# Kernel tuning notes

Hardware: AMD Instinct MI355X
Metric: run time of the kernel (lower is better)

Reference implementation:

```python
import jax, jax.numpy as jnp
import numpy as np
from jax import lax

# dims
B, T, C, V, L = 4, 1024, 1024, 32000, 2
NR, NT, E = 6, 2, 8          # rwkv experts, transformer experts, total
HID = 4 * C                  # FFN hidden
P, R = 8, 64                 # bridge prefix_len, low_rank_dim
NH, HD = 16, 64              # heads, head_size


def _layernorm(x, g, b, eps=1e-5):
    m = jnp.mean(x, axis=-1, keepdims=True)
    v = jnp.var(x, axis=-1, keepdims=True)
    return (x - m) * lax.rsqrt(v + eps) * g + b


def setup_inputs() -> dict:
    key = jax.random.key(0)
    ks = list(jax.random.split(key, 32))
    it = iter(ks)
    def nrm(shape, s=0.02):
        return jax.random.normal(next(it), shape, dtype=jnp.float32) * s
    inp = {}
    inp['idx'] = jax.random.randint(next(it), (B, T), 0, V)
    inp['capital_shares'] = jax.random.uniform(next(it), (L, E), dtype=jnp.float32)
    inp['emb'] = nrm((V, C), 1.0)
    inp['head'] = nrm((C, V))
    inp['ln1_g'] = jnp.ones((L, C), jnp.float32)
    inp['ln1_b'] = jnp.zeros((L, C), jnp.float32)
    inp['ln2_g'] = jnp.ones((L, C), jnp.float32)
    inp['ln2_b'] = jnp.zeros((L, C), jnp.float32)
    inp['lno_g'] = jnp.ones((C,), jnp.float32)
    inp['lno_b'] = jnp.zeros((C,), jnp.float32)
    inp['att_Wr'] = nrm((L, C, C))
    inp['att_Wk'] = nrm((L, C, C))
    inp['att_Wv'] = nrm((L, C, C))
    inp['att_Wo'] = nrm((L, C, C))
    inp['att_decay'] = nrm((L, C), 1.0)
    inp['critic_wd'] = nrm((L, C))
    inp['critic_Wa'] = nrm((L, C, E))
    inp['bridge_Wdown'] = nrm((C, R))
    inp['bridge_Wup'] = nrm((P, R, C))
    inp['eWk'] = nrm((L, NR, C, HID))
    inp['eWv'] = nrm((L, NR, HID, C))
    inp['conf_r'] = nrm((L, NR, C))
    inp['tWq'] = nrm((L, NT, C, C))
    inp['tWk'] = nrm((L, NT, C, C))
    inp['tWv'] = nrm((L, NT, C, C))
    inp['tWo'] = nrm((L, NT, C, C))
    inp['conf_t'] = nrm((L, NT, C))
    return inp


def _forward(idx, capital_shares, emb, head, ln1_g, ln1_b, ln2_g, ln2_b,
             lno_g, lno_b, att_Wr, att_Wk, att_Wv, att_Wo, att_decay,
             critic_wd, critic_Wa, bridge_Wdown, bridge_Wup,
             eWk, eWv, conf_r, tWq, tWk, tWv, tWo, conf_t):
    x = emb[idx]                                   # [B,T,C]
    v_first = jnp.zeros_like(x)
    for l in range(L):
        # --- TimeMix (simplified RWKV: per-channel decayed kv state) ---
        x_ln = _layernorm(x, ln1_g[l], ln1_b[l])
        r = jax.nn.sigmoid(x_ln @ att_Wr[l])       # [B,T,C]
        k = x_ln @ att_Wk[l]
        v = x_ln @ att_Wv[l]
        if l == 0:
            v_first = v
        else:
            v = 0.5 * (v + v_first)
        w = jax.nn.sigmoid(att_decay[l])           # [C] decay in (0,1)
        def step(s, kv):
            kt, vt = kv
            s = w * s + kt * vt
            return s, s
        kT = jnp.swapaxes(k, 0, 1)                 # [T,B,C]
        vT = jnp.swapaxes(v, 0, 1)
        _, s_seq = lax.scan(step, jnp.zeros((B, C), x.dtype), (kT, vT))
        rwkv_state = jnp.swapaxes(s_seq, 0, 1)     # [B,T,C]
        att_out = (r * rwkv_state) @ att_Wo[l]
        x = x + att_out
        # --- routing (market) ---
        h = _layernorm(x, ln2_g[l], ln2_b[l])
        conf_rw = jax.nn.sigmoid(jnp.einsum('btc,ec->bte', h, conf_r[l]))
        conf_tr = jax.nn.sigmoid(jnp.einsum('btc,ec->bte', h, conf_t[l]))
        confidences = jnp.concatenate([conf_rw, conf_tr], axis=-1)  # [B,T,E]
        difficulty = jax.nn.softplus(jnp.einsum('btc,c->bt', h, critic_wd[l]))[..., None]
        affinity = jnp.einsum('btc,ce->bte', h, critic_Wa[l])
        subsidy = jnp.tanh(affinity)               # critic.apply_to_bids(0, affinity)
        bids = confidences * capital_shares[l] * difficulty + subsidy
        top2_vals, winners = lax.top_k(bids, 2)    # [B,T,2]
        weights = jax.nn.softmax(top2_vals, axis=-1)
        gate = (weights[..., 0:1] * jax.nn.one_hot(winners[..., 0], E, dtype=h.dtype)
                + weights[..., 1:2] * jax.nn.one_hot(winners[..., 1], E, dtype=h.dtype))  # [B,T,E]
        # --- bridge prefix (low-rank, shared) ---
        flat_h = h.reshape(-1, C)
        flat_state = rwkv_state.reshape(-1, C)
        u = (flat_h + flat_state) @ bridge_Wdown   # [N,R]
        prefix = jnp.einsum('nr,prc->npc', u, bridge_Wup)  # [N,P,C]
        # --- experts: dense-equivalent of gather/compute/scatter ---
        final = jnp.zeros_like(h)
        for e in range(NR):                        # squared-relu FFN experts
            hid = jnp.square(jax.nn.relu(h @ eWk[l, e]))
            final = final + gate[..., e:e + 1] * (hid @ eWv[l, e])
        scale = 1.0 / jnp.sqrt(jnp.float32(HD))
        for j in range(NT):                        # linear transformer experts over prefix
            q = (flat_h @ tWq[l, j]).reshape(-1, NH, HD)
            kp = (prefix @ tWk[l, j]).reshape(-1, P, NH, HD)
            vp = (prefix @ tWv[l, j]).reshape(-1, P, NH, HD)
            attn = jax.nn.softmax(jnp.einsum('nhd,nphd->nhp', q, kp) * scale, axis=-1)
            o = jnp.einsum('nhp,nphd->nhd', attn, vp).reshape(-1, C) @ tWo[l, j]
            final = final + gate[..., NR + j:NR + j + 1] * o.reshape(B, T, C)
        x = x + final
    x = _layernorm(x, lno_g, lno_b)
    return x @ head                                # [B,T,V] logits


def reference(idx, capital_shares, emb, head, ln1_g, ln1_b, ln2_g, ln2_b,
              lno_g, lno_b, att_Wr, att_Wk, att_Wv, att_Wo, att_decay,
              critic_wd, critic_Wa, bridge_Wdown, bridge_Wup,
              eWk, eWv, conf_r, tWq, tWk, tWv, tWo, conf_t):
    return _forward(idx, capital_shares, emb, head, ln1_g, ln1_b, ln2_g, ln2_b,
                    lno_g, lno_b, att_Wr, att_Wk, att_Wv, att_Wo, att_decay,
                    critic_wd, critic_Wa, bridge_Wdown, bridge_Wup,
                    eWk, eWv, conf_r, tWq, tWk, tWv, tWo, conf_t)
```

## Files before the change

### kernel.cpp

```cpp
#include <hip/hip_runtime.h>

typedef _Float16 h16;
typedef __attribute__((ext_vector_type(8))) _Float16 h16x8;
typedef __attribute__((ext_vector_type(4))) _Float16 h16x4;
typedef __attribute__((ext_vector_type(4))) float f32x4;

#define DEVFN static __device__ __forceinline__

DEVFN void gl_lds16(const void* g, void* l) {
  __builtin_amdgcn_global_load_lds((const __attribute__((address_space(1))) unsigned int*)g,
                                   (__attribute__((address_space(3))) unsigned int*)l, 16, 0, 0);
}
DEVFN void fsplit(float v, h16& hi, h16& lo) { hi = (h16)v; lo = (h16)(v - (float)hi); }
DEVFN float wred(float v) {
  #pragma unroll
  for (int m = 32; m >= 1; m >>= 1) v += __shfl_xor(v, m, 64);
  return v;
}
DEVFN float sigm(float x) { return 1.0f / (1.0f + expf(-x)); }
DEVFN float softpl(float x) { return fmaxf(x, 0.0f) + log1pf(expf(-fabsf(x))); }

enum { EPI_WRITE = 0, EPI_ADD = 1, EPI_SQRELU = 3, EPI_TSPLIT = 4, EPI_SCATTER = 5 };

template<bool SPLIT, int EPI, int MODE>
__global__ __launch_bounds__(256, 2) void gemm_k(
    const h16* __restrict__ Ah, const h16* __restrict__ Al, long lda, long sAz,
    const h16* __restrict__ Bh, const h16* __restrict__ Bl, long ldb, long sBz,
    float* __restrict__ C, long ldc, long sCz,
    h16* __restrict__ Oh, h16* __restrict__ Ol, long ldo,
    int K, int nmask, const float* __restrict__ rs, int rsStride,
    const int4* __restrict__ meta, int metaStep,
    const int* __restrict__ lists, int listStep)
{
  __shared__ h16 As[(SPLIT ? 2 : 1) * 4096];
  __shared__ h16 Bs[(SPLIT ? 2 : 1) * 4096];
  const int tid = threadIdx.x;
  const int lane = tid & 63, wave = tid >> 6;
  const int wr = wave >> 1, wc = wave & 1;
  const long z = blockIdx.z;
  const long m0 = (long)blockIdx.x * 128, n0 = (long)blockIdx.y * 128;

  int cntv = 0;
  long koff = 0;
  const int* lst = nullptr;
  if (MODE == 1) {
    const int4 mt = meta[z * metaStep];
    if ((int)m0 >= mt.y) return;
    cntv = mt.x; lst = lists + z * listStep;
  } else if (MODE == 2) {
    const int4 mt = meta[0];
    if ((int)m0 >= mt.y) return;
    cntv = mt.x; lst = lists; koff = z * (long)K;
  }

  const h16* pAh = Ah + z * sAz;
  const h16* pBh = Bh + z * sBz;
  const h16* pAl = SPLIT ? (Al + z * sAz) : nullptr;
  const h16* pBl = SPLIT ? (Bl + z * sBz) : nullptr;
  const int rA = wave * 16 + (lane >> 2);
  const int khalf = (lane & 3) * 8;
  long arow0, arow1;
  if (MODE == 1) { arow0 = lst[m0 + rA]; arow1 = lst[m0 + rA + 64]; }
  else           { arow0 = m0 + rA; arow1 = arow0 + 64; }
  const long aoff0 = arow0 * lda + khalf + koff;
  const long aoff1 = arow1 * lda + khalf + koff;
  const long boff = (n0 + rA) * ldb + khalf + koff;
  h16* lA = &As[wave * 512];
  h16* lB = &Bs[wave * 512];
  const int fr = lane & 15, fq = lane >> 4;

  const f32x4 zero = {0.f, 0.f, 0.f, 0.f};
  f32x4 acc[4][4];
  #pragma unroll
  for (int m = 0; m < 4; m++)
    #pragma unroll
    for (int n = 0; n < 4; n++) acc[m][n] = zero;

  for (int k0 = 0; k0 < K; k0 += 32) {
    gl_lds16(pAh + aoff0 + k0, lA);
    gl_lds16(pAh + aoff1 + k0, lA + 2048);
    gl_lds16(pBh + boff + k0, lB);
    gl_lds16(pBh + boff + k0 + 64 * ldb, lB + 2048);
    if (SPLIT) {
      gl_lds16(pAl + aoff0 + k0, lA + 4096);
      gl_lds16(pAl + aoff1 + k0, lA + 4096 + 2048);
      gl_lds16(pBl + boff + k0, lB + 4096);
      gl_lds16(pBl + boff + k0 + 64 * ldb, lB + 4096 + 2048);
    }
    __syncthreads();
    h16x8 af[4], bf[4], afl[4], bfl[4];
    #pragma unroll
    for (int m = 0; m < 4; m++) {
      const int r = (wr * 64 + m * 16 + fr) * 32 + fq * 8;
      af[m] = *(const h16x8*)&As[r];
      if (SPLIT) afl[m] = *(const h16x8*)&As[4096 + r];
    }
    #pragma unroll
    for (int n = 0; n < 4; n++) {
      const int r = (wc * 64 + n * 16 + fr) * 32 + fq * 8;
      bf[n] = *(const h16x8*)&Bs[r];
      if (SPLIT) bfl[n] = *(const h16x8*)&Bs[4096 + r];
    }
    #pragma unroll
    for (int m = 0; m < 4; m++)
      #pragma unroll
      for (int n = 0; n < 4; n++) {
        acc[m][n] = __builtin_amdgcn_mfma_f32_16x16x32_f16(af[m], bf[n], acc[m][n], 0, 0, 0);
        if (SPLIT) {
          acc[m][n] = __builtin_amdgcn_mfma_f32_16x16x32_f16(af[m], bfl[n], acc[m][n], 0, 0, 0);
          acc[m][n] = __builtin_amdgcn_mfma_f32_16x16x32_f16(afl[m], bf[n], acc[m][n], 0, 0, 0);
        }
      }
    __syncthreads();
  }

  #pragma unroll
  for (int m = 0; m < 4; m++) {
    const long lrow = m0 + wr * 64 + m * 16 + fq * 4;
    #pragma unroll
    for (int n = 0; n < 4; n++) {
      const long gcol = n0 + wc * 64 + n * 16 + fr;
      if (nmask && gcol >= nmask) continue;
      if (EPI == EPI_TSPLIT) {
        h16x4 hv, lv;
        #pragma unroll
        for (int i = 0; i < 4; i++) { h16 a, b2; fsplit(acc[m][n][i], a, b2); hv[i] = a; lv[i] = b2; }
        *(h16x4*)&Oh[gcol * ldo + lrow] = hv;
        *(h16x4*)&Ol[gcol * ldo + lrow] = lv;
      } else if (EPI == EPI_SCATTER) {
        #pragma unroll
        for (int i = 0; i < 4; i++) {
          const int slot = (int)lrow + i;
          if (slot >= cntv) continue;
          const int tok = lst[slot];
          const float g = rs[(long)tok * rsStride];
          atomicAdd(&C[(long)tok * ldc + gcol], g * acc[m][n][i]);
        }
      } else {
        float* cp = C + z * sCz + lrow * ldc + gcol;
        #pragma unroll
        for (int i = 0; i < 4; i++) {
          const float v = acc[m][n][i];
          if (EPI == EPI_WRITE) cp[i * ldc] = v;
          else cp[i * ldc] += v;
        }
      }
    }
  }
}

template<bool SPLIT, int EPI, int MODE>
__global__ __launch_bounds__(512, 1) void gemm256_k(
    const h16* __restrict__ Ah, const h16* __restrict__ Al, long lda,
    const h16* __restrict__ Bh, const h16* __restrict__ Bl, long ldb, long sBz,
    float* __restrict__ C, long ldc,
    h16* __restrict__ Oh, h16* __restrict__ Ol, long ldo,
    int K, const float* __restrict__ rs, int rsStride,
    const int4* __restrict__ meta, const int* __restrict__ lists, int listStep,
    const int* __restrict__ mmap)
{
  __shared__ h16 As[(SPLIT ? 2 : 1) * 8192];
  __shared__ h16 Bs[(SPLIT ? 2 : 1) * 8192];
  const int tid = threadIdx.x;
  const int lane = tid & 63, wave = tid >> 6;
  const int wr = wave >> 2, wc = wave & 3;
  const long m0 = (long)blockIdx.x * 256, n0 = (long)blockIdx.y * 256;

  int cntv = 0, eIdx = 0, eOff = 0;
  long koff = 0;
  const int* lst = nullptr;
  if (MODE == 3 || MODE == 4) {
    if ((int)m0 >= meta[8].x) return;
    eIdx = mmap[blockIdx.x];
    const int4 mt = meta[eIdx];
    cntv = mt.x; eOff = mt.z;
    lst = lists + eIdx * listStep;
    if (MODE == 4) koff = blockIdx.z * (long)K;
  }

  const h16* pAh = Ah;
  const h16* pBh = Bh + (long)eIdx * sBz;
  const h16* pAl = SPLIT ? Al : nullptr;
  const h16* pBl = SPLIT ? (Bl + (long)eIdx * sBz) : nullptr;
  const int rA = (tid >> 2) & 127;
  const int khalf = (lane & 3) * 8;
  long arow0, arow1;
  if (MODE == 3) { arow0 = lst[m0 + rA - eOff]; arow1 = lst[m0 + rA + 128 - eOff]; }
  else           { arow0 = m0 + rA; arow1 = arow0 + 128; }
  const long aoff0 = arow0 * lda + khalf + koff;
  const long aoff1 = arow1 * lda + khalf + koff;
  const long boff0 = (n0 + rA) * ldb + khalf + koff;
  const long boff1 = boff0 + 128 * ldb;
  h16* lA = &As[wave * 512];
  h16* lB = &Bs[wave * 512];
  const int fr = lane & 15, fq = lane >> 4;

  const f32x4 zero = {0.f, 0.f, 0.f, 0.f};
  f32x4 acc[8][4];
  #pragma unroll
  for (int m = 0; m < 8; m++)
    #pragma unroll
    for (int n = 0; n < 4; n++) acc[m][n] = zero;

  for (int k0 = 0; k0 < K; k0 += 32) {
    gl_lds16(pAh + aoff0 + k0, lA);
    gl_lds16(pAh + aoff1 + k0, lA + 4096);
    gl_lds16(pBh + boff0 + k0, lB);
    gl_lds16(pBh + boff1 + k0, lB + 4096);
    if (SPLIT) {
      gl_lds16(pAl + aoff0 + k0, lA + 8192);
      gl_lds16(pAl + aoff1 + k0, lA + 8192 + 4096);
      gl_lds16(pBl + boff0 + k0, lB + 8192);
      gl_lds16(pBl + boff1 + k0, lB + 8192 + 4096);
    }
    __syncthreads();
    h16x8 bf[4], bfl[4];
    #pragma unroll
    for (int n = 0; n < 4; n++) {
      const int r = (wc * 64 + n * 16 + fr) * 32 + fq * 8;
      bf[n] = *(const h16x8*)&Bs[r];
      if (SPLIT) bfl[n] = *(const h16x8*)&Bs[8192 + r];
    }
    #pragma unroll
    for (int m = 0; m < 8; m++) {
      const int r = (wr * 128 + m * 16 + fr) * 32 + fq * 8;
      const h16x8 af = *(const h16x8*)&As[r];
      h16x8 afl;
      if (SPLIT) afl = *(const h16x8*)&As[8192 + r];
      #pragma unroll
      for (int n = 0; n < 4; n++) {
        acc[m][n] = __builtin_amdgcn_mfma_f32_16x16x32_f16(af, bf[n], acc[m][n], 0, 0, 0);
        if (SPLIT) {
          acc[m][n] = __builtin_amdgcn_mfma_f32_16x16x32_f16(af, bfl[n], acc[m][n], 0, 0, 0);
          acc[m][n] = __builtin_amdgcn_mfma_f32_16x16x32_f16(afl, bf[n], acc[m][n], 0, 0, 0);
        }
      }
    }
    __syncthreads();
  }

  #pragma unroll
  for (int m = 0; m < 8; m++) {
    const long lrow = m0 + wr * 128 + m * 16 + fq * 4;
    #pragma unroll
    for (int n = 0; n < 4; n++) {
      const long gcol = n0 + wc * 64 + n * 16 + fr;
      if (EPI == EPI_SQRELU) {
        #pragma unroll
        for (int i = 0; i < 4; i++) {
          float v = acc[m][n][i];
          v = v > 0.f ? v * v : 0.f;
          const h16 a = (h16)v;
          Oh[(lrow + i) * ldo + gcol] = a;
          if (Ol) Ol[(lrow + i) * ldo + gcol] = (h16)(v - (float)a);
        }
      } else if (EPI == EPI_SCATTER) {
        #pragma unroll
        for (int i = 0; i < 4; i++) {
          const int slot = (int)lrow + i - eOff;
          if (slot >= cntv) continue;
          const int tok = lst[slot];
          atomicAdd(&C[(long)tok * ldc + gcol], rs[(long)tok * rsStride + eIdx] * acc[m][n][i]);
        }
      } else {
        float* cp = C + lrow * ldc + gcol;
        #pragma unroll
        for (int i = 0; i < 4; i++) cp[i * ldc] = acc[m][n][i];
      }
    }
  }
}

template<bool LO>
__global__ __launch_bounds__(256) void k_tsplit(
    const float* __restrict__ in, long inZ,
    h16* __restrict__ oh, h16* __restrict__ ol, long outZ, int Kd, int Nd)
{
  __shared__ float t[64][65];
  const long z = blockIdx.z;
  in += z * inZ; oh += z * outZ; if (LO) ol += z * outZ;
  const int n0 = blockIdx.x * 64, k0 = blockIdx.y * 64;
  const int tr = threadIdx.x >> 4, tc = threadIdx.x & 15;
  #pragma unroll
  for (int r = 0; r < 4; r++) {
    const int row = r * 16 + tr;
    const float4 v = *(const float4*)&in[(long)(k0 + row) * Nd + n0 + tc * 4];
    t[row][tc * 4 + 0] = v.x; t[row][tc * 4 + 1] = v.y;
    t[row][tc * 4 + 2] = v.z; t[row][tc * 4 + 3] = v.w;
  }
  __syncthreads();
  #pragma unroll
  for (int r = 0; r < 4; r++) {
    const int nrow = r * 16 + tr;
    h16x4 hv, lv;
    #pragma unroll
    for (int i = 0; i < 4; i++) {
      h16 a, b2; fsplit(t[tc * 4 + i][nrow], a, b2);
      hv[i] = a; lv[i] = b2;
    }
    *(h16x4*)&oh[(long)(n0 + nrow) * Kd + k0 + tc * 4] = hv;
    if (LO) *(h16x4*)&ol[(long)(n0 + nrow) * Kd + k0 + tc * 4] = lv;
  }
}

__global__ void k_split(const float* __restrict__ in, h16* __restrict__ oh, h16* __restrict__ ol)
{
  const long i = (long)blockIdx.x * 256 + threadIdx.x;
  const float4 v = ((const float4*)in)[i];
  h16x4 hv, lv; h16 a, b2;
  fsplit(v.x, a, b2); hv[0] = a; lv[0] = b2;
  fsplit(v.y, a, b2); hv[1] = a; lv[1] = b2;
  fsplit(v.z, a, b2); hv[2] = a; lv[2] = b2;
  fsplit(v.w, a, b2); hv[3] = a; lv[3] = b2;
  ((h16x4*)oh)[i] = hv; ((h16x4*)ol)[i] = lv;
}

__global__ void k_embed(const int* __restrict__ idx, const float* __restrict__ emb, float* __restrict__ x)
{
  const int row = blockIdx.x;
  const long e = (long)idx[row] * 1024;
  ((float4*)(x + (long)row * 1024))[threadIdx.x] = ((const float4*)(emb + e))[threadIdx.x];
}

__global__ __launch_bounds__(256) void k_ln(
    const float* __restrict__ x, const float* __restrict__ g, const float* __restrict__ b,
    float* __restrict__ yf, h16* __restrict__ yh, h16* __restrict__ yl)
{
  const int row = blockIdx.x, tid = threadIdx.x;
  const float4 v = ((const float4*)(x + (long)row * 1024))[tid];
  __shared__ float red[4];
  const int wv = tid >> 6;
  float s = wred(v.x + v.y + v.z + v.w);
  if ((tid & 63) == 0) red[wv] = s;
  __syncthreads();
  const float mean = (red[0] + red[1] + red[2] + red[3]) * (1.0f / 1024.0f);
  const float d0 = v.x - mean, d1 = v.y - mean, d2 = v.z - mean, d3 = v.w - mean;
  float s2 = wred(d0 * d0 + d1 * d1 + d2 * d2 + d3 * d3);
  __syncthreads();
  if ((tid & 63) == 0) red[wv] = s2;
  __syncthreads();
  const float var = (red[0] + red[1] + red[2] + red[3]) * (1.0f / 1024.0f);
  const float rstd = 1.0f / sqrtf(var + 1e-5f);
  const float4 gv = ((const float4*)g)[tid];
  const float4 bv = ((const float4*)b)[tid];
  const float y0 = d0 * rstd * gv.x + bv.x;
  const float y1 = d1 * rstd * gv.y + bv.y;
  const float y2 = d2 * rstd * gv.z + bv.z;
  const float y3 = d3 * rstd * gv.w + bv.w;
  if (yf) { float4 o; o.x = y0; o.y = y1; o.z = y2; o.w = y3; ((float4*)(yf + (long)row * 1024))[tid] = o; }
  h16x4 hv, lv; h16 a, b2;
  fsplit(y0, a, b2); hv[0] = a; lv[0] = b2;
  fsplit(y1, a, b2); hv[1] = a; lv[1] = b2;
  fsplit(y2, a, b2); hv[2] = a; lv[2] = b2;
  fsplit(y3, a, b2); hv[3] = a; lv[3] = b2;
  *(h16x4*)(yh + (long)row * 1024 + tid * 4) = hv;
  if (yl) *(h16x4*)(yl + (long)row * 1024 + tid * 4) = lv;
}

__global__ void k_vfix(float* __restrict__ rkv, float* __restrict__ vfir, int mode)
{
  const int row = blockIdx.x, tid = threadIdx.x;
  float4* vp = (float4*)(rkv + (long)row * 3072 + 2048) + tid;
  float4* fp = (float4*)(vfir + (long)row * 1024) + tid;
  if (mode == 0) *fp = *vp;
  else {
    float4 a = *vp; const float4 b = *fp;
    a.x = 0.5f * (a.x + b.x); a.y = 0.5f * (a.y + b.y);
    a.z = 0.5f * (a.z + b.z); a.w = 0.5f * (a.w + b.w);
    *vp = a;
  }
}

__global__ __launch_bounds__(256) void k_scan1(const float* __restrict__ rkv,
                                               const float* __restrict__ dec, float* __restrict__ carry)
{
  const int gid = blockIdx.x * 256 + threadIdx.x;
  const int c = gid & 1023, bb = (gid >> 10) & 3, ch = gid >> 12;
  const float w = sigm(dec[c]);
  float s = 0.f;
  const long base = ((long)bb * 1024 + ch * 64) * 3072 + c;
  const float* kp_ = rkv + 1024 + base;
  const float* vp_ = rkv + 2048 + base;
  for (int t = 0; t < 64; t++) s = w * s + kp_[(long)t * 3072] * vp_[(long)t * 3072];
  carry[(ch * 4 + bb) * 1024 + c] = s;
}
__global__ void k_scan2(const float* __restrict__ dec, float* __restrict__ carry)
{
  const int gid = blockIdx.x * 256 + threadIdx.x;
  const int c = gid & 1023, bb = gid >> 10;
  const float w = sigm(dec[c]);
  float w64 = w;
  for (int i = 0; i < 6; i++) w64 *= w64;
  float s = 0.f;
  for (int j = 0; j < 16; j++) {
    const int o = (j * 4 + bb) * 1024 + c;
    const float a = carry[o];
    carry[o] = s;
    s = w64 * s + a;
  }
}
__global__ __launch_bounds__(256) void k_scan3(const float* __restrict__ rkv,
                                               const float* __restrict__ dec, const float* __restrict__ carry,
                                               float* __restrict__ st)
{
  const int gid = blockIdx.x * 256 + threadIdx.x;
  const int c = gid & 1023, bb = (gid >> 10) & 3, ch = gid >> 12;
  const float w = sigm(dec[c]);
  float s = carry[(ch * 4 + bb) * 1024 + c];
  const long base = ((long)bb * 1024 + ch * 64) * 3072 + c;
  const float* kp_ = rkv + 1024 + base;
  const float* vp_ = rkv + 2048 + base;
  float* so = st + ((long)bb * 1024 + ch * 64) * 1024 + c;
  for (int t = 0; t < 64; t++) {
    s = w * s + kp_[(long)t * 3072] * vp_[(long)t * 3072];
    so[(long)t * 1024] = s;
  }
}

__global__ void k_attin(const float* __restrict__ rkv, const float* __restrict__ s,
                        h16* __restrict__ oh, h16* __restrict__ ol)
{
  const int row = blockIdx.x, tid = threadIdx.x;
  const float4 rv = *((const float4*)(rkv + (long)row * 3072) + tid);
  const float4 sv = *((const float4*)(s + (long)row * 1024) + tid);
  h16x4 hv, lv; h16 a, b2;
  fsplit(sv.x * sigm(rv.x), a, b2); hv[0] = a; lv[0] = b2;
  fsplit(sv.y * sigm(rv.y), a, b2); hv[1] = a; lv[1] = b2;
  fsplit(sv.z * sigm(rv.z), a, b2); hv[2] = a; lv[2] = b2;
  fsplit(sv.w * sigm(rv.w), a, b2); hv[3] = a; lv[3] = b2;
  const long i = (long)row * 256 + tid;
  ((h16x4*)oh)[i] = hv; ((h16x4*)ol)[i] = lv;
}

__global__ void k_addsplit(const float* __restrict__ p, const float* __restrict__ q,
                           h16* __restrict__ oh, h16* __restrict__ ol)
{
  const long i = (long)blockIdx.x * 256 + threadIdx.x;
  const float4 av = ((const float4*)p)[i];
  const float4 bv = ((const float4*)q)[i];
  h16x4 hv, lv; h16 a, b2;
  fsplit(av.x + bv.x, a, b2); hv[0] = a; lv[0] = b2;
  fsplit(av.y + bv.y, a, b2); hv[1] = a; lv[1] = b2;
  fsplit(av.z + bv.z, a, b2); hv[2] = a; lv[2] = b2;
  fsplit(av.w + bv.w, a, b2); hv[3] = a; lv[3] = b2;
  ((h16x4*)oh)[i] = hv; ((h16x4*)ol)[i] = lv;
}

__global__ __launch_bounds__(256) void k_route(
    const float* __restrict__ h, const float* __restrict__ cr, const float* __restrict__ ct,
    const float* __restrict__ wd, const float* __restrict__ wa,
    const float* __restrict__ cap, float* __restrict__ gate)
{
  const int wv = threadIdx.x >> 6, ln = threadIdx.x & 63;
  const int row = blockIdx.x * 4 + wv;
  const float* hr = h + (long)row * 1024;
  float hreg[16];
  #pragma unroll
  for (int i = 0; i < 4; i++) {
    const float4 t = ((const float4*)hr)[ln * 4 + i];
    hreg[i * 4 + 0] = t.x; hreg[i * 4 + 1] = t.y; hreg[i * 4 + 2] = t.z; hreg[i * 4 + 3] = t.w;
  }
  float dots[17];
  #pragma unroll
  for (int e = 0; e < 6; e++) {
    float p = 0.f;
    #pragma unroll
    for (int j = 0; j < 16; j++) p += hreg[j] * cr[e * 1024 + ln * 16 + j];
    dots[e] = p;
  }
  #pragma unroll
  for (int e = 0; e < 2; e++) {
    float p = 0.f;
    #pragma unroll
    for (int j = 0; j < 16; j++) p += hreg[j] * ct[e * 1024 + ln * 16 + j];
    dots[6 + e] = p;
  }
  {
    float p = 0.f;
    #pragma unroll
    for (int j = 0; j < 16; j++) p += hreg[j] * wd[ln * 16 + j];
    dots[8] = p;
  }
  #pragma unroll
  for (int e = 0; e < 8; e++) {
    float p = 0.f;
    #pragma unroll
    for (int j = 0; j < 16; j++) p += hreg[j] * wa[(ln * 16 + j) * 8 + e];
    dots[9 + e] = p;
  }
  #pragma unroll
  for (int d = 0; d < 17; d++) dots[d] = wred(dots[d]);
  if (ln == 0) {
    float bids[8];
    const float diff = softpl(dots[8]);
    #pragma unroll
    for (int e = 0; e < 6; e++) bids[e] = sigm(dots[e]) * cap[e] * diff + tanhf(dots[9 + e]);
    #pragma unroll
    for (int e = 0; e < 2; e++) bids[6 + e] = sigm(dots[6 + e]) * cap[6 + e] * diff + tanhf(dots[15 + e]);
    int w0 = 0;
    for (int e = 1; e < 8; e++) if (bids[e] > bids[w0]) w0 = e;
    int w1 = -1;
    for (int e = 0; e < 8; e++) if (e != w0 && (w1 < 0 || bids[e] > bids[w1])) w1 = e;
    const float e1 = expf(bids[w1] - bids[w0]);
    const float q0 = 1.0f / (1.0f + e1), q1 = e1 / (1.0f + e1);
    for (int e = 0; e < 8; e++) gate[(long)row * 8 + e] = (e == w0) ? q0 : ((e == w1) ? q1 : 0.0f);
  }
}

__global__ void k_build(const float* __restrict__ gate, int* __restrict__ cnt, int* __restrict__ lists)
{
  const int t = blockIdx.x * 256 + threadIdx.x;
  #pragma unroll
  for (int e = 0; e < 8; e++)
    if (gate[(long)t * 8 + e] > 0.f) { const int s = atomicAdd(&cnt[e], 1); lists[e * 4224 + s] = t; }
}
__global__ void k_meta(const int* __restrict__ cnt, int4* __restrict__ meta, int* __restrict__ lists,
                       int* __restrict__ mmap)
{
  __shared__ int sc[8], sp[8], so[8];
  if (threadIdx.x == 0) {
    int acc = 0;
    for (int e = 0; e < 8; e++) {
      const int c = cnt[e], p = (c + 255) & ~255;
      sc[e] = c; sp[e] = p; so[e] = (e < 6) ? acc : 0;
      if (e < 6) acc += p;
    }
    meta[8] = make_int4(acc, 0, 0, 0);
    for (int b = 0; b < 64; b++) mmap[b] = 0;
    for (int e = 0; e < 6; e++)
      for (int b = so[e] >> 8; b < (so[e] + sp[e]) >> 8; b++) mmap[b] = e;
  }
  __syncthreads();
  const int e = threadIdx.x >> 5, i = threadIdx.x & 31;
  for (int s = sc[e] + i; s < sp[e]; s += 32) lists[e * 4224 + s] = 0;
  if (i == 0) meta[e] = make_int4(sc[e], sp[e], so[e], 0);
}

__global__ __launch_bounds__(256) void k_scores(const float* __restrict__ q, const float* __restrict__ kp,
                                                float* __restrict__ attn, const int4* __restrict__ meta)
{
  const int gw = blockIdx.x * 4 + (threadIdx.x >> 6), ln = threadIdx.x & 63;
  const int n = gw >> 4, hh = gw & 15;
  if (n >= meta->y) return;
  const float qv = q[(long)n * 1024 + hh * 64 + ln];
  float s[8];
  #pragma unroll
  for (int p = 0; p < 8; p++) {
    float t = qv * kp[(long)n * 8192 + p * 1024 + hh * 64 + ln];
    s[p] = wred(t) * 0.125f;
  }
  if (ln == 0) {
    float mx = s[0];
    #pragma unroll
    for (int p = 1; p < 8; p++) mx = fmaxf(mx, s[p]);
    float ex[8], sum = 0.f;
    #pragma unroll
    for (int p = 0; p < 8; p++) { ex[p] = expf(s[p] - mx); sum += ex[p]; }
    const float inv = 1.0f / sum;
    #pragma unroll
    for (int p = 0; p < 8; p++) attn[(long)n * 128 + hh * 8 + p] = ex[p] * inv;
  }
}

__global__ void k_omix(const float* __restrict__ attn, const float* __restrict__ vp,
                       h16* __restrict__ oh, h16* __restrict__ ol, const int4* __restrict__ meta)
{
  const long gid = (long)blockIdx.x * 256 + threadIdx.x;
  const int n = gid >> 10, hd = gid & 1023, hh = hd >> 6;
  if (n >= meta->y) return;
  const float* a = attn + (long)n * 128 + hh * 8;
  float o = 0.f;
  #pragma unroll
  for (int p = 0; p < 8; p++) o += a[p] * vp[(long)n * 8192 + p * 1024 + hd];
  h16 hi, lo; fsplit(o, hi, lo);
  oh[gid] = hi; ol[gid] = lo;
}

#define GEMM3(SPL, EPI, MODE, GRID, ...) do { \
  if (SPL) gemm_k<true,  EPI, MODE><<<GRID, 256, 0, stream>>>(__VA_ARGS__); \
  else     gemm_k<false, EPI, MODE><<<GRID, 256, 0, stream>>>(__VA_ARGS__); } while (0)
#define GEMM256(SPL, EPI, MODE, GRID, ...) do { \
  if (SPL) gemm256_k<true,  EPI, MODE><<<GRID, 512, 0, stream>>>(__VA_ARGS__); \
  else     gemm256_k<false, EPI, MODE><<<GRID, 512, 0, stream>>>(__VA_ARGS__); } while (0)

extern "C" void kernel_launch(void* const* d_in, const int* in_sizes, int n_in,
                              void* d_out, int out_size, void* d_ws, size_t ws_size,
                              hipStream_t stream)
{
  (void)in_sizes; (void)n_in; (void)out_size; (void)ws_size;
  const int*   idx   = (const int*)  d_in[0];
  const float* cap   = (const float*)d_in[1];
  const float* emb   = (const float*)d_in[2];
  const float* headw = (const float*)d_in[3];
  const float* ln1g  = (const float*)d_in[4];
  const float* ln1b  = (const float*)d_in[5];
  const float* ln2g  = (const float*)d_in[6];
  const float* ln2b  = (const float*)d_in[7];
  const float* lnog  = (const float*)d_in[8];
  const float* lnob  = (const float*)d_in[9];
  const float* aWr   = (const float*)d_in[10];
  const float* aWk   = (const float*)d_in[11];
  const float* aWv   = (const float*)d_in[12];
  const float* aWo   = (const float*)d_in[13];
  const float* adec  = (const float*)d_in[14];
  const float* cwd   = (const float*)d_in[15];
  const float* cWa   = (const float*)d_in[16];
  const float* bWd   = (const float*)d_in[17];
  const float* bWu   = (const float*)d_in[18];
  const float* eWkw  = (const float*)d_in[19];
  const float* eWvw  = (const float*)d_in[20];
  const float* confr = (const float*)d_in[21];
  const float* tWq   = (const float*)d_in[22];
  const float* tWkk  = (const float*)d_in[23];
  const float* tWv   = (const float*)d_in[24];
  const float* tWo   = (const float*)d_in[25];
  const float* conft = (const float*)d_in[26];
  float* out = (float*)d_out;

  char* ws = (char*)d_ws;
  size_t off = 0;
  auto alloc = [&](size_t n) -> char* {
    off = (off + 255) & ~(size_t)255;
    char* p = ws + off; off += n; return p;
  };
  const long M1 = 1048576, M4 = 4194304;

  h16* attWh = (h16*)alloc(8 * M1 * 2);
  h16* attWl = (h16*)alloc(8 * M1 * 2);
  h16* eWkh  = (h16*)alloc(12 * M4 * 2);
  h16* eWkl  = (h16*)alloc(6 * M4 * 2);
  h16* eWvh  = (h16*)alloc(12 * M4 * 2);
  h16* eWvl  = (h16*)alloc(6 * M4 * 2);
  h16* tWh   = (h16*)alloc(16 * M1 * 2);
  h16* tWl   = (h16*)alloc(8 * M1 * 2);
  h16* headh = (h16*)alloc(32768000ull * 2);
  h16* wdh   = (h16*)alloc(131072 * 2);
  h16* wdl   = (h16*)alloc(131072 * 2);
  h16* wuph  = (h16*)alloc(524288 * 2);
  h16* wupl  = (h16*)alloc(524288 * 2);
  h16* wukth = (h16*)alloc(524288 * 2);
  h16* wuktl = (h16*)alloc(524288 * 2);
  h16* wuvth = (h16*)alloc(524288 * 2);
  h16* wuvtl = (h16*)alloc(524288 * 2);
  h16* s1h   = (h16*)alloc(M4 * 2);
  h16* s1l   = (h16*)alloc(M4 * 2);
  h16* hh_   = (h16*)alloc(M4 * 2);
  h16* hl_   = (h16*)alloc(M4 * 2);
  h16* uh    = (h16*)alloc(262144 * 2);
  h16* ul    = (h16*)alloc(262144 * 2);
  float* x    = (float*)alloc(M4 * 4);
  float* vfir = (float*)alloc(M4 * 4);
  float* rkv  = (float*)alloc(3 * M4 * 4);
  float* st   = (float*)alloc(M4 * 4);
  float* hf   = (float*)alloc(M4 * 4);
  float* qf   = (float*)alloc(M4 * 4);
  char* big   = alloc(167772160);
  h16* hidh   = (h16*)big;
  h16* hidl   = (h16*)(big + 83886080ull);
  float* kp   = (float*)big;
  float* carry = (float*)alloc(65536 * 4);
  float* gate  = (float*)alloc(32768 * 4);
  float* uf    = (float*)alloc(262144 * 4);
  float* attn  = (float*)alloc(524288 * 4);
  int*   cnt8  = (int*)alloc(32);
  int4*  metaA = (int4*)alloc(16 * 16);
  int*   lists = (int*)alloc(8 * 4224 * 4);
  int*   mmap  = (int*)alloc(64 * 4);

  const float* aW[4] = {aWr, aWk, aWv, aWo};
  for (int w = 0; w < 4; w++)
    k_tsplit<true><<<dim3(16, 16, 2), 256, 0, stream>>>(aW[w], M1, attWh + w * M1, attWl + w * M1, 4 * M1, 1024, 1024);
  k_tsplit<true ><<<dim3(64, 16, 6), 256, 0, stream>>>(eWkw, M4, eWkh, eWkl, M4, 1024, 4096);
  k_tsplit<false><<<dim3(64, 16, 6), 256, 0, stream>>>(eWkw + 6 * M4, M4, eWkh + 6 * M4, nullptr, M4, 1024, 4096);
  k_tsplit<true ><<<dim3(16, 64, 6), 256, 0, stream>>>(eWvw, M4, eWvh, eWvl, M4, 4096, 1024);
  k_tsplit<false><<<dim3(16, 64, 6), 256, 0, stream>>>(eWvw + 6 * M4, M4, eWvh + 6 * M4, nullptr, M4, 4096, 1024);
  const float* tWsrc[4] = {tWq, tWkk, tWv, tWo};
  for (int m = 0; m < 4; m++) {
    k_tsplit<true ><<<dim3(16, 16, 2), 256, 0, stream>>>(tWsrc[m], M1, tWh + m * M1, tWl + m * M1, 4 * M1, 1024, 1024);
    k_tsplit<false><<<dim3(16, 16, 2), 256, 0, stream>>>(tWsrc[m] + 2 * M1, M1, tWh + (8 + m) * M1, nullptr, 4 * M1, 1024, 1024);
  }
  k_tsplit<false><<<dim3(500, 16, 1), 256, 0, stream>>>(headw, 0, headh, nullptr, 0, 1024, 32000);
  k_tsplit<true ><<<dim3(1, 16, 1), 256, 0, stream>>>(bWd, 0, wdh, wdl, 0, 1024, 64);
  hipMemsetAsync(wdh + 65536, 0, 65536 * 2, stream);
  hipMemsetAsync(wdl + 65536, 0, 65536 * 2, stream);
  k_split<<<512, 256, 0, stream>>>(bWu, wuph, wupl);

  k_embed<<<4096, 256, 0, stream>>>(idx, emb, x);

  for (int l = 0; l < 2; l++) {
    const bool SE = (l == 0);
    k_ln<<<4096, 256, 0, stream>>>(x, ln1g + l * 1024, ln1b + l * 1024, nullptr, s1h, s1l);
    GEMM3(true, EPI_WRITE, 0, dim3(32, 24),
          s1h, s1l, 1024, 0, attWh + (l * 4) * M1, attWl + (l * 4) * M1, 1024, 0,
          rkv, 3072, 0, nullptr, nullptr, 0, 1024, 0, nullptr, 0, nullptr, 0, nullptr, 0);
    k_vfix<<<4096, 256, 0, stream>>>(rkv, vfir, l == 0 ? 0 : 1);
    k_scan1<<<256, 256, 0, stream>>>(rkv, adec + l * 1024, carry);
    k_scan2<<<16, 256, 0, stream>>>(adec + l * 1024, carry);
    k_scan3<<<256, 256, 0, stream>>>(rkv, adec + l * 1024, carry, st);
    k_attin<<<4096, 256, 0, stream>>>(rkv, st, s1h, s1l);
    GEMM3(true, EPI_ADD, 0, dim3(32, 8),
          s1h, s1l, 1024, 0, attWh + (l * 4 + 3) * M1, attWl + (l * 4 + 3) * M1, 1024, 0,
          x, 1024, 0, nullptr, nullptr, 0, 1024, 0, nullptr, 0, nullptr, 0, nullptr, 0);
    k_ln<<<4096, 256, 0, stream>>>(x, ln2g + l * 1024, ln2b + l * 1024, hf, hh_, hl_);
    k_route<<<1024, 256, 0, stream>>>(hf, confr + l * 6144, conft + l * 2048, cwd + l * 1024, cWa + l * 8192, cap + l * 8, gate);
    hipMemsetAsync(cnt8, 0, 32, stream);
    k_build<<<16, 256, 0, stream>>>(gate, cnt8, lists);
    k_meta<<<1, 256, 0, stream>>>(cnt8, metaA, lists, mmap);
    k_addsplit<<<4096, 256, 0, stream>>>(hf, st, s1h, s1l);
    GEMM3(true, EPI_WRITE, 0, dim3(32, 1),
          s1h, s1l, 1024, 0, wdh, wdl, 1024, 0,
          uf, 64, 0, nullptr, nullptr, 0, 1024, 64, nullptr, 0, nullptr, 0, nullptr, 0);
    k_split<<<256, 256, 0, stream>>>(uf, uh, ul);
    GEMM256(SE, EPI_SQRELU, 3, dim3(40, 16),
            hh_, hl_, 1024, eWkh + l * 6 * M4, eWkl, 1024, M4,
            nullptr, 0, hidh, SE ? hidl : nullptr, 4096,
            1024, nullptr, 0, metaA, lists, 4224, mmap);
    GEMM256(SE, EPI_SCATTER, 4, dim3(40, 4, 4),
            hidh, hidl, 4096, eWvh + l * 6 * M4, eWvl, 4096, M4,
            x, 1024, nullptr, nullptr, 0,
            1024, gate, 8, metaA, lists, 4224, mmap);
    for (int j = 0; j < 2; j++) {
      const long wi = (l * 2 + j) * 4, wl = j * 4;
      const int4* mt = metaA + 6 + j;
      const int* lstT = lists + (6 + j) * 4224;
      GEMM3(SE, EPI_TSPLIT, 0, dim3(4, 8),
            wuph, wupl, 1024, 0, tWh + (wi + 1) * M1, tWl + (wl + 1) * M1, 1024, 0,
            nullptr, 0, 0, wukth, wuktl, 512, 1024, 0, nullptr, 0, nullptr, 0, nullptr, 0);
      GEMM3(SE, EPI_TSPLIT, 0, dim3(4, 8),
            wuph, wupl, 1024, 0, tWh + (wi + 2) * M1, tWl + (wl + 2) * M1, 1024, 0,
            nullptr, 0, 0, wuvth, wuvtl, 512, 1024, 0, nullptr, 0, nullptr, 0, nullptr, 0);
      GEMM3(SE, EPI_WRITE, 1, dim3(32, 8),
            hh_, hl_, 1024, 0, tWh + (wi + 0) * M1, tWl + (wl + 0) * M1, 1024, 0,
            qf, 1024, 0, nullptr, nullptr, 0, 1024, 0, nullptr, 0, mt, 0, lstT, 0);
      GEMM3(SE, EPI_WRITE, 1, dim3(32, 8, 8),
            uh, ul, 64, 0, wukth, wuktl, 512, 64,
            kp, 8192, 1024, nullptr, nullptr, 0, 64, 0, nullptr, 0, mt, 0, lstT, 0);
      k_scores<<<16384, 256, 0, stream>>>(qf, kp, attn, mt);
      GEMM3(SE, EPI_WRITE, 1, dim3(32, 8, 8),
            uh, ul, 64, 0, wuvth, wuvtl, 512, 64,
            kp, 8192, 1024, nullptr, nullptr, 0, 64, 0, nullptr, 0, mt, 0, lstT, 0);
      k_omix<<<16384, 256, 0, stream>>>(attn, kp, s1h, s1l, mt);
      GEMM3(SE, EPI_SCATTER, 2, dim3(32, 8, 4),
            s1h, s1l, 1024, 0, tWh + (wi + 3) * M1, tWl + (wl + 3) * M1, 1024, 0,
            x, 1024, 0, nullptr, nullptr, 0, 256, 0, gate + 6 + j, 8, mt, 0, lstT, 0);
    }
  }

  k_ln<<<4096, 256, 0, stream>>>(x, lnog, lnob, nullptr, s1h, s1l);
  GEMM3(false, EPI_WRITE, 0, dim3(32, 250),
        s1h, nullptr, 1024, 0, headh, nullptr, 1024, 0,
        out, 32000, 0, nullptr, nullptr, 0, 1024, 0, nullptr, 0, nullptr, 0, nullptr, 0);
}
```

Baseline: 3.367 ms.

## Drop split-fp16 precision on transformer-expert and bridge GEMMs, batch weight conversions

Switches the transformer-expert GEMMs (q, key/value prefix projections, output scatter) and the bridge down-projection from the 3-MFMA hi/lo split-precision path to a single fp16 pass, removing the low-part weights entirely. The two prefix-projection TSPLIT GEMMs are merged into one launch using a new z-stride on the output, with the wukth/wuvth buffers reordered so they are contiguous. Weight preprocessing for the attention and transformer weights is batched into single k_tsplit4 launches. This cuts MFMA work and launches, at the cost of reduced numerical accuracy in those paths.

```diff
diff --git a/kernel.cpp b/kernel.cpp
--- a/kernel.cpp
+++ b/kernel.cpp
@@ -30,7 +30,7 @@
     h16* __restrict__ Oh, h16* __restrict__ Ol, long ldo,
     int K, int nmask, const float* __restrict__ rs, int rsStride,
     const int4* __restrict__ meta, int metaStep,
-    const int* __restrict__ lists, int listStep)
+    const int* __restrict__ lists, int listStep, long sOz)
 {
   __shared__ h16 As[(SPLIT ? 2 : 1) * 4096];
   __shared__ h16 Bs[(SPLIT ? 2 : 1) * 4096];
@@ -125,8 +125,8 @@
         h16x4 hv, lv;
         #pragma unroll
         for (int i = 0; i < 4; i++) { h16 a, b2; fsplit(acc[m][n][i], a, b2); hv[i] = a; lv[i] = b2; }
-        *(h16x4*)&Oh[gcol * ldo + lrow] = hv;
-        *(h16x4*)&Ol[gcol * ldo + lrow] = lv;
+        *(h16x4*)&Oh[z * sOz + gcol * ldo + lrow] = hv;
+        *(h16x4*)&Ol[z * sOz + gcol * ldo + lrow] = lv;
       } else if (EPI == EPI_SCATTER) {
         #pragma unroll
         for (int i = 0; i < 4; i++) {
@@ -279,6 +279,42 @@
   __shared__ float t[64][65];
   const long z = blockIdx.z;
   in += z * inZ; oh += z * outZ; if (LO) ol += z * outZ;
+  const int n0 = blockIdx.x * 64, k0 = blockIdx.y * 64;
+  const int tr = threadIdx.x >> 4, tc = threadIdx.x & 15;
+  #pragma unroll
+  for (int r = 0; r < 4; r++) {
+    const int row = r * 16 + tr;
+    const float4 v = *(const float4*)&in[(long)(k0 + row) * Nd + n0 + tc * 4];
+    t[row][tc * 4 + 0] = v.x; t[row][tc * 4 + 1] = v.y;
+    t[row][tc * 4 + 2] = v.z; t[row][tc * 4 + 3] = v.w;
+  }
+  __syncthreads();
+  #pragma unroll
+  for (int r = 0; r < 4; r++) {
+    const int nrow = r * 16 + tr;
+    h16x4 hv, lv;
+    #pragma unroll
+    for (int i = 0; i < 4; i++) {
+      h16 a, b2; fsplit(t[tc * 4 + i][nrow], a, b2);
+      hv[i] = a; lv[i] = b2;
+    }
+    *(h16x4*)&oh[(long)(n0 + nrow) * Kd + k0 + tc * 4] = hv;
+    if (LO) *(h16x4*)&ol[(long)(n0 + nrow) * Kd + k0 + tc * 4] = lv;
+  }
+}
+
+template<bool LO>
+__global__ __launch_bounds__(256) void k_tsplit4(
+    const float* __restrict__ s0, const float* __restrict__ s1,
+    const float* __restrict__ s2, const float* __restrict__ s3,
+    long inAdd, h16* __restrict__ oh, h16* __restrict__ ol, int Kd, int Nd)
+{
+  __shared__ float t[64][65];
+  const int z = blockIdx.z;
+  const long seg = (long)Kd * Nd;
+  const int w = z & 3;
+  const float* in = (w == 0 ? s0 : w == 1 ? s1 : w == 2 ? s2 : s3) + (inAdd + (z >> 2)) * seg;
+  oh += (long)z * seg; if (LO) ol += (long)z * seg;
   const int n0 = blockIdx.x * 64, k0 = blockIdx.y * 64;
   const int tr = threadIdx.x >> 4, tc = threadIdx.x & 15;
   #pragma unroll
@@ -632,15 +668,13 @@
   h16* eWvh  = (h16*)alloc(12 * M4 * 2);
   h16* eWvl  = (h16*)alloc(6 * M4 * 2);
   h16* tWh   = (h16*)alloc(16 * M1 * 2);
-  h16* tWl   = (h16*)alloc(8 * M1 * 2);
   h16* headh = (h16*)alloc(32768000ull * 2);
   h16* wdh   = (h16*)alloc(131072 * 2);
-  h16* wdl   = (h16*)alloc(131072 * 2);
   h16* wuph  = (h16*)alloc(524288 * 2);
   h16* wupl  = (h16*)alloc(524288 * 2);
   h16* wukth = (h16*)alloc(524288 * 2);
+  h16* wuvth = (h16*)alloc(524288 * 2);
   h16* wuktl = (h16*)alloc(524288 * 2);
-  h16* wuvth = (h16*)alloc(524288 * 2);
   h16* wuvtl = (h16*)alloc(524288 * 2);
   h16* s1h   = (h16*)alloc(M4 * 2);
   h16* s1l   = (h16*)alloc(M4 * 2);
@@ -667,22 +701,15 @@
   int*   lists = (int*)alloc(8 * 4224 * 4);
   int*   mmap  = (int*)alloc(64 * 4);
 
-  const float* aW[4] = {aWr, aWk, aWv, aWo};
-  for (int w = 0; w < 4; w++)
-    k_tsplit<true><<<dim3(16, 16, 2), 256, 0, stream>>>(aW[w], M1, attWh + w * M1, attWl + w * M1, 4 * M1, 1024, 1024);
+  k_tsplit4<true><<<dim3(16, 16, 8), 256, 0, stream>>>(aWr, aWk, aWv, aWo, 0, attWh, attWl, 1024, 1024);
   k_tsplit<true ><<<dim3(64, 16, 6), 256, 0, stream>>>(eWkw, M4, eWkh, eWkl, M4, 1024, 4096);
   k_tsplit<false><<<dim3(64, 16, 6), 256, 0, stream>>>(eWkw + 6 * M4, M4, eWkh + 6 * M4, nullptr, M4, 1024, 4096);
   k_tsplit<true ><<<dim3(16, 64, 6), 256, 0, stream>>>(eWvw, M4, eWvh, eWvl, M4, 4096, 1024);
   k_tsplit<false><<<dim3(16, 64, 6), 256, 0, stream>>>(eWvw + 6 * M4, M4, eWvh + 6 * M4, nullptr, M4, 4096, 1024);
-  const float* tWsrc[4] = {tWq, tWkk, tWv, tWo};
-  for (int m = 0; m < 4; m++) {
-    k_tsplit<true ><<<dim3(16, 16, 2), 256, 0, stream>>>(tWsrc[m], M1, tWh + m * M1, tWl + m * M1, 4 * M1, 1024, 1024);
-    k_tsplit<false><<<dim3(16, 16, 2), 256, 0, stream>>>(tWsrc[m] + 2 * M1, M1, tWh + (8 + m) * M1, nullptr, 4 * M1, 1024, 1024);
-  }
+  k_tsplit4<false><<<dim3(16, 16, 16), 256, 0, stream>>>(tWq, tWkk, tWv, tWo, 0, tWh, nullptr, 1024, 1024);
   k_tsplit<false><<<dim3(500, 16, 1), 256, 0, stream>>>(headw, 0, headh, nullptr, 0, 1024, 32000);
-  k_tsplit<true ><<<dim3(1, 16, 1), 256, 0, stream>>>(bWd, 0, wdh, wdl, 0, 1024, 64);
+  k_tsplit<false><<<dim3(1, 16, 1), 256, 0, stream>>>(bWd, 0, wdh, nullptr, 0, 1024, 64);
   hipMemsetAsync(wdh + 65536, 0, 65536 * 2, stream);
-  hipMemsetAsync(wdl + 65536, 0, 65536 * 2, stream);
   k_split<<<512, 256, 0, stream>>>(bWu, wuph, wupl);
 
   k_embed<<<4096, 256, 0, stream>>>(idx, emb, x);
@@ -692,7 +719,7 @@
     k_ln<<<4096, 256, 0, stream>>>(x, ln1g + l * 1024, ln1b + l * 1024, nullptr, s1h, s1l);
     GEMM3(true, EPI_WRITE, 0, dim3(32, 24),
           s1h, s1l, 1024, 0, attWh + (l * 4) * M1, attWl + (l * 4) * M1, 1024, 0,
-          rkv, 3072, 0, nullptr, nullptr, 0, 1024, 0, nullptr, 0, nullptr, 0, nullptr, 0);
+          rkv, 3072, 0, nullptr, nullptr, 0, 1024, 0, nullptr, 0, nullptr, 0, nullptr, 0, 0);
     k_vfix<<<4096, 256, 0, stream>>>(rkv, vfir, l == 0 ? 0 : 1);
     k_scan1<<<256, 256, 0, stream>>>(rkv, adec + l * 1024, carry);
     k_scan2<<<16, 256, 0, stream>>>(adec + l * 1024, carry);
@@ -700,16 +727,16 @@
     k_attin<<<4096, 256, 0, stream>>>(rkv, st, s1h, s1l);
     GEMM3(true, EPI_ADD, 0, dim3(32, 8),
           s1h, s1l, 1024, 0, attWh + (l * 4 + 3) * M1, attWl + (l * 4 + 3) * M1, 1024, 0,
-          x, 1024, 0, nullptr, nullptr, 0, 1024, 0, nullptr, 0, nullptr, 0, nullptr, 0);
+          x, 1024, 0, nullptr, nullptr, 0, 1024, 0, nullptr, 0, nullptr, 0, nullptr, 0, 0);
     k_ln<<<4096, 256, 0, stream>>>(x, ln2g + l * 1024, ln2b + l * 1024, hf, hh_, hl_);
     k_route<<<1024, 256, 0, stream>>>(hf, confr + l * 6144, conft + l * 2048, cwd + l * 1024, cWa + l * 8192, cap + l * 8, gate);
     hipMemsetAsync(cnt8, 0, 32, stream);
     k_build<<<16, 256, 0, stream>>>(gate, cnt8, lists);
     k_meta<<<1, 256, 0, stream>>>(cnt8, metaA, lists, mmap);
     k_addsplit<<<4096, 256, 0, stream>>>(hf, st, s1h, s1l);
-    GEMM3(true, EPI_WRITE, 0, dim3(32, 1),
-          s1h, s1l, 1024, 0, wdh, wdl, 1024, 0,
-          uf, 64, 0, nullptr, nullptr, 0, 1024, 64, nullptr, 0, nullptr, 0, nullptr, 0);
+    GEMM3(false, EPI_WRITE, 0, dim3(32, 1),
+          s1h, nullptr, 1024, 0, wdh, nullptr, 1024, 0,
+          uf, 64, 0, nullptr, nullptr, 0, 1024, 64, nullptr, 0, nullptr, 0, nullptr, 0, 0);
     k_split<<<256, 256, 0, stream>>>(uf, uh, ul);
     GEMM256(SE, EPI_SQRELU, 3, dim3(40, 16),
             hh_, hl_, 1024, eWkh + l * 6 * M4, eWkl, 1024, M4,
@@ -720,34 +747,31 @@
             x, 1024, nullptr, nullptr, 0,
             1024, gate, 8, metaA, lists, 4224, mmap);
     for (int j = 0; j < 2; j++) {
-      const long wi = (l * 2 + j) * 4, wl = j * 4;
+      const long wi = (l * 2 + j) * 4;
       const int4* mt = metaA + 6 + j;
       const int* lstT = lists + (6 + j) * 4224;
-      GEMM3(SE, EPI_TSPLIT, 0, dim3(4, 8),
-            wuph, wupl, 1024, 0, tWh + (wi + 1) * M1, tWl + (wl + 1) * M1, 1024, 0,
-            nullptr, 0, 0, wukth, wuktl, 512, 1024, 0, nullptr, 0, nullptr, 0, nullptr, 0);
-      GEMM3(SE, EPI_TSPLIT, 0, dim3(4, 8),
-            wuph, wupl, 1024, 0, tWh + (wi + 2) * M1, tWl + (wl + 2) * M1, 1024, 0,
-            nullptr, 0, 0, wuvth, wuvtl, 512, 1024, 0, nullptr, 0, nullptr, 0, nullptr, 0);
-      GEMM3(SE, EPI_WRITE, 1, dim3(32, 8),
-            hh_, hl_, 1024, 0, tWh + (wi + 0) * M1, tWl + (wl + 0) * M1, 1024, 0,
-            qf, 1024, 0, nullptr, nullptr, 0, 1024, 0, nullptr, 0, mt, 0, lstT, 0);
-      GEMM3(SE, EPI_WRITE, 1, dim3(32, 8, 8),
-            uh, ul, 64, 0, wukth, wuktl, 512, 64,
-            kp, 8192, 1024, nullptr, nullptr, 0, 64, 0, nullptr, 0, mt, 0, lstT, 0);
+      GEMM3(false, EPI_TSPLIT, 0, dim3(4, 8, 2),
+            wuph, nullptr, 1024, 0, tWh + (wi + 1) * M1, nullptr, 1024, M1,
+            nullptr, 0, 0, wukth, wuktl, 512, 1024, 0, nullptr, 0, nullptr, 0, nullptr, 0, 524288);
+      GEMM3(false, EPI_WRITE, 1, dim3(32, 8),
+            hh_, nullptr, 1024, 0, tWh + (wi + 0) * M1, nullptr, 1024, 0,
+            qf, 1024, 0, nullptr, nullptr, 0, 1024, 0, nullptr, 0, mt, 0, lstT, 0, 0);
+      GEMM3(false, EPI_WRITE, 1, dim3(32, 8, 8),
+            uh, nullptr, 64, 0, wukth, nullptr, 512, 64,
+            kp, 8192, 1024, nullptr, nullptr, 0, 64, 0, nullptr, 0, mt, 0, lstT, 0, 0);
       k_scores<<<16384, 256, 0, stream>>>(qf, kp, attn, mt);
-      GEMM3(SE, EPI_WRITE, 1, dim3(32, 8, 8),
-            uh, ul, 64, 0, wuvth, wuvtl, 512, 64,
-            kp, 8192, 1024, nullptr, nullptr, 0, 64, 0, nullptr, 0, mt, 0, lstT, 0);
+      GEMM3(false, EPI_WRITE, 1, dim3(32, 8, 8),
+            uh, nullptr, 64, 0, wuvth, nullptr, 512, 64,
+            kp, 8192, 1024, nullptr, nullptr, 0, 64, 0, nullptr, 0, mt, 0, lstT, 0, 0);
       k_omix<<<16384, 256, 0, stream>>>(attn, kp, s1h, s1l, mt);
-      GEMM3(SE, EPI_SCATTER, 2, dim3(32, 8, 4),
-            s1h, s1l, 1024, 0, tWh + (wi + 3) * M1, tWl + (wl + 3) * M1, 1024, 0,
-            x, 1024, 0, nullptr, nullptr, 0, 256, 0, gate + 6 + j, 8, mt, 0, lstT, 0);
+      GEMM3(false, EPI_SCATTER, 2, dim3(32, 8, 4),
+            s1h, nullptr, 1024, 0, tWh + (wi + 3) * M1, nullptr, 1024, 0,
+            x, 1024, 0, nullptr, nullptr, 0, 256, 0, gate + 6 + j, 8, mt, 0, lstT, 0, 0);
     }
   }
 
   k_ln<<<4096, 256, 0, stream>>>(x, lnog, lnob, nullptr, s1h, s1l);
   GEMM3(false, EPI_WRITE, 0, dim3(32, 250),
         s1h, nullptr, 1024, 0, headh, nullptr, 1024, 0,
-        out, 32000, 0, nullptr, nullptr, 0, 1024, 0, nullptr, 0, nullptr, 0, nullptr, 0);
-}
+        out, 32000, 0, nullptr, nullptr, 0, 1024, 0, nullptr, 0, nullptr, 0, nullptr, 0, 0);
+}
```

Measured after the change: 2.954 ms. -12.3%, faster.
